# Optimization experiments

Measured on AMD Instinct MI355X. Metric: run time of the kernel, lower is better.

Reference implementation:

```python
import jax, jax.numpy as jnp
import numpy as np

KW, KH = 8, 8   # kernel_size = (kw, kh) per torch module indexing
SW, SH = 4, 4   # stride_size = (sw, sh)


def setup_inputs() -> dict:
    key = jax.random.key(0)
    x = jax.random.normal(key, (4, 128, 128, 128), dtype=jnp.float32)  # [B, C, H, W]
    return {"x": x}


def _local_autocorr(x, kh=KH, kw=KW, sh=SH, sw=SW):
    B, C, H, W = x.shape
    nh = (H - kh) // sh + 1
    nw = (W - kw) // sw + 1
    # Background is x zero-padded by (kh//2, (kh+1)//2 - 1) vertically and
    # (kw//2, (kw+1)//2 - 1) horizontally -> background patches are (2kh-1, 2kw-1).
    xp = jnp.pad(x, ((0, 0), (0, 0),
                     (kh // 2, (kh + 1) // 2 - 1),
                     (kw // 2, (kw + 1) // 2 - 1)))

    # For each shift (dy, dx) in [0,kh)x[0,kw):
    #   ret[b,iy,ix,c,dy,dx] = sum_{u,v} x[b,c,top+u,left+v] * xp[b,c,top+dy+u,left+dx+v]
    # i.e. elementwise product with the shifted map, then sum-pool with window (kh,kw), stride (sh,sw).
    def step(carry, s):
        dy = s // kw
        dx = s % kw
        shifted = jax.lax.dynamic_slice(xp, (0, 0, dy, dx), (B, C, H, W))
        prod = x * shifted
        pooled = jax.lax.reduce_window(prod, 0.0, jax.lax.add,
                                       (1, 1, kh, kw), (1, 1, sh, sw), 'VALID')
        return carry, pooled  # [B, C, nh, nw]

    _, stacked = jax.lax.scan(step, None, jnp.arange(kh * kw))
    # stacked: [kh*kw, B, C, nh, nw] with shift index s = dy*kw + dx
    out = stacked.reshape(kh, kw, B, C, nh, nw)
    out = jnp.transpose(out, (2, 4, 5, 3, 0, 1))  # [B, nh, nw, C, kh, kw]
    return out


def reference(x):
    return _local_autocorr(x)
```

## Files before the change

kernel.cpp:

```cpp
#include <hip/hip_runtime.h>


#define Cn 128
#define Hn 128
#define Wn 128
#define NH 31
#define NW 31
#define CB 4
#define PXT 8
#define PYT 4
#define TROWS 27
#define RST 44
#define CST (TROWS*RST)
#define F4C (TROWS*11)
#define TCST 17
#define TPST (CB*TCST+1)

__global__ __launch_bounds__(256, 2)
void lac_kernel(const float* __restrict__ x, float* __restrict__ out) {
    __shared__ float sm[CB * CST];

    const int bid = blockIdx.x;
    const int lg = ((bid & 7) << 9) | (bid >> 3);
    const int tx = lg & 3;
    const int ty = (lg >> 2) & 7;
    const int ct = (lg >> 5) & 31;
    const int b  = lg >> 10;
    const int c0 = ct * CB;
    const int gy0 = ty * (PYT * 4) - 4;
    const int gx0 = tx * (PXT * 4) - 4;
    const int tid = threadIdx.x;

    for (int i = tid; i < CB * F4C; i += 256) {
        const int c   = i / F4C;
        const int rem = i - c * F4C;
        const int r   = rem / 11;
        const int q   = rem - r * 11;
        const int y   = gy0 + r;
        const int xc  = gx0 + q * 4;
        const float* src = x + (((size_t)(b * Cn + c0 + c) * Hn + y) * Wn + xc);
        float4 v;
        if (y >= 0 && y < Hn && xc >= 0 && xc + 3 < Wn) {
            v = *reinterpret_cast<const float4*>(src);
        } else if (y >= 0 && y < Hn) {
            v.x = (xc + 0 >= 0 && xc + 0 < Wn) ? src[0] : 0.0f;
            v.y = (xc + 1 >= 0 && xc + 1 < Wn) ? src[1] : 0.0f;
            v.z = (xc + 2 >= 0 && xc + 2 < Wn) ? src[2] : 0.0f;
            v.w = (xc + 3 >= 0 && xc + 3 < Wn) ? src[3] : 0.0f;
        } else {
            v = make_float4(0.0f, 0.0f, 0.0f, 0.0f);
        }
        reinterpret_cast<float4*>(sm)[i] = v;
    }
    __syncthreads();

    const int cs   = tid & 3;
    const int px   = (tid >> 2) & 7;
    const int py   = (tid >> 5) & 3;
    const int half = tid >> 7;
    const float* rg  = &sm[cs * CST + (py * 4) * RST + px * 4];
    const float* rgr = rg + (half * 4) * RST;

    float acc[4][8];
#pragma unroll
    for (int i = 0; i < 4; ++i)
#pragma unroll
        for (int j = 0; j < 8; ++j) acc[i][j] = 0.0f;

#pragma unroll
    for (int rr = 0; rr < 11; ++rr) {
        float rw[16];
        float4 q0 = *reinterpret_cast<const float4*>(&rgr[rr * RST + 0]);
        float4 q1 = *reinterpret_cast<const float4*>(&rgr[rr * RST + 4]);
        float4 q2 = *reinterpret_cast<const float4*>(&rgr[rr * RST + 8]);
        float4 q3 = *reinterpret_cast<const float4*>(&rgr[rr * RST + 12]);
        rw[0]  = q0.x; rw[1]  = q0.y; rw[2]  = q0.z; rw[3]  = q0.w;
        rw[4]  = q1.x; rw[5]  = q1.y; rw[6]  = q1.z; rw[7]  = q1.w;
        rw[8]  = q2.x; rw[9]  = q2.y; rw[10] = q2.z; rw[11] = q2.w;
        rw[12] = q3.x; rw[13] = q3.y; rw[14] = q3.z; rw[15] = q3.w;
#pragma unroll
        for (int d = 0; d < 4; ++d) {
            const int u = rr - d;
            if (u >= 0 && u < 8) {
                float4 b0 = *reinterpret_cast<const float4*>(&rg[(u + 4) * RST + 4]);
                float4 b1 = *reinterpret_cast<const float4*>(&rg[(u + 4) * RST + 8]);
                float bsr[8];
                bsr[0] = b0.x; bsr[1] = b0.y; bsr[2] = b0.z; bsr[3] = b0.w;
                bsr[4] = b1.x; bsr[5] = b1.y; bsr[6] = b1.z; bsr[7] = b1.w;
#pragma unroll
                for (int v = 0; v < 8; ++v) {
                    const float bv = bsr[v];
#pragma unroll
                    for (int dx = 0; dx < 8; ++dx)
                        acc[d][dx] = fmaf(bv, rw[v + dx], acc[d][dx]);
                }
            }
        }
    }

    float4* lds4 = reinterpret_cast<float4*>(sm);
#pragma unroll
    for (int rnd = 0; rnd < 4; ++rnd) {
        __syncthreads();
        if (py == rnd) {
            const int wb = px * TPST + cs * TCST + half * 8;
#pragma unroll
            for (int d = 0; d < 4; ++d) {
                lds4[wb + d * 2 + 0] = make_float4(acc[d][0], acc[d][1], acc[d][2], acc[d][3]);
                lds4[wb + d * 2 + 1] = make_float4(acc[d][4], acc[d][5], acc[d][6], acc[d][7]);
            }
        }
        __syncthreads();
        const int iy = ty * PYT + rnd;
        if (iy < NH) {
#pragma unroll
            for (int sp = 0; sp < 2; ++sp) {
                const int p  = sp * 4 + (tid >> 6);
                const int ix = tx * PXT + p;
                if (ix < NW) {
                    const int j = tid & 63;
                    float4* obase = reinterpret_cast<float4*>(
                        out + ((((size_t)b * NH + iy) * NW + ix) * Cn + c0) * 64);
                    obase[j] = lds4[p * TPST + (j >> 4) * TCST + (j & 15)];
                }
            }
        }
    }
}

extern "C" void kernel_launch(void* const* d_in, const int* in_sizes, int n_in,
                              void* d_out, int out_size, void* d_ws, size_t ws_size,
                              hipStream_t stream) {
    const float* x = (const float*)d_in[0];
    float* out = (float*)d_out;
    lac_kernel<<<dim3(4096), dim3(256), 0, stream>>>(x, out);
}
```

Before: 101.4 us.

## Reuse loaded background rows as kernel rows via register ring buffer

```diff
diff --git a/kernel.cpp b/kernel.cpp
--- a/kernel.cpp
+++ b/kernel.cpp
@@ -11,14 +11,14 @@
 #define PYT 4
 #define TROWS 27
 #define RST 44
-#define CST (TROWS*RST)
+#define CSTF4 310
 #define F4C (TROWS*11)
 #define TCST 17
 #define TPST (CB*TCST+1)
 
 __global__ __launch_bounds__(256, 2)
 void lac_kernel(const float* __restrict__ x, float* __restrict__ out) {
-    __shared__ float sm[CB * CST];
+    __shared__ float sm[CB * CSTF4 * 4];
 
     const int bid = blockIdx.x;
     const int lg = ((bid & 7) << 9) | (bid >> 3);
@@ -50,7 +50,7 @@
         } else {
             v = make_float4(0.0f, 0.0f, 0.0f, 0.0f);
         }
-        reinterpret_cast<float4*>(sm)[i] = v;
+        reinterpret_cast<float4*>(sm)[c * CSTF4 + r * 11 + q] = v;
     }
     __syncthreads();
 
@@ -58,8 +58,7 @@
     const int px   = (tid >> 2) & 7;
     const int py   = (tid >> 5) & 3;
     const int half = tid >> 7;
-    const float* rg  = &sm[cs * CST + (py * 4) * RST + px * 4];
-    const float* rgr = rg + (half * 4) * RST;
+    const float* rg = &sm[cs * (CSTF4 * 4) + (py * 4) * RST + px * 4];
 
     float acc[4][8];
 #pragma unroll
@@ -67,36 +66,63 @@
 #pragma unroll
         for (int j = 0; j < 8; ++j) acc[i][j] = 0.0f;
 
+    float ks[4][8];
+
+#define LOAD_RW(R)                                                              \
+    float rw[16];                                                               \
+    {                                                                           \
+        float4 q0 = *reinterpret_cast<const float4*>(&rg[(R) * RST + 0]);       \
+        float4 q1 = *reinterpret_cast<const float4*>(&rg[(R) * RST + 4]);       \
+        float4 q2 = *reinterpret_cast<const float4*>(&rg[(R) * RST + 8]);       \
+        float4 q3 = *reinterpret_cast<const float4*>(&rg[(R) * RST + 12]);      \
+        rw[0]=q0.x; rw[1]=q0.y; rw[2]=q0.z; rw[3]=q0.w;                         \
+        rw[4]=q1.x; rw[5]=q1.y; rw[6]=q1.z; rw[7]=q1.w;                         \
+        rw[8]=q2.x; rw[9]=q2.y; rw[10]=q2.z; rw[11]=q2.w;                       \
+        rw[12]=q3.x; rw[13]=q3.y; rw[14]=q3.z; rw[15]=q3.w;                     \
+    }
+
+    if (half == 0) {
 #pragma unroll
-    for (int rr = 0; rr < 11; ++rr) {
-        float rw[16];
-        float4 q0 = *reinterpret_cast<const float4*>(&rgr[rr * RST + 0]);
-        float4 q1 = *reinterpret_cast<const float4*>(&rgr[rr * RST + 4]);
-        float4 q2 = *reinterpret_cast<const float4*>(&rgr[rr * RST + 8]);
-        float4 q3 = *reinterpret_cast<const float4*>(&rgr[rr * RST + 12]);
-        rw[0]  = q0.x; rw[1]  = q0.y; rw[2]  = q0.z; rw[3]  = q0.w;
-        rw[4]  = q1.x; rw[5]  = q1.y; rw[6]  = q1.z; rw[7]  = q1.w;
-        rw[8]  = q2.x; rw[9]  = q2.y; rw[10] = q2.z; rw[11] = q2.w;
-        rw[12] = q3.x; rw[13] = q3.y; rw[14] = q3.z; rw[15] = q3.w;
+        for (int ii = 0; ii < 12; ++ii) {
+            const int R = 11 - ii;
+            LOAD_RW(R)
 #pragma unroll
-        for (int d = 0; d < 4; ++d) {
-            const int u = rr - d;
-            if (u >= 0 && u < 8) {
-                float4 b0 = *reinterpret_cast<const float4*>(&rg[(u + 4) * RST + 4]);
-                float4 b1 = *reinterpret_cast<const float4*>(&rg[(u + 4) * RST + 8]);
-                float bsr[8];
-                bsr[0] = b0.x; bsr[1] = b0.y; bsr[2] = b0.z; bsr[3] = b0.w;
-                bsr[4] = b1.x; bsr[5] = b1.y; bsr[6] = b1.z; bsr[7] = b1.w;
+            for (int d = 0; d < 4; ++d) {
+                if (R >= d && R <= 7 + d) {
 #pragma unroll
-                for (int v = 0; v < 8; ++v) {
-                    const float bv = bsr[v];
+                    for (int v = 0; v < 8; ++v) {
+                        const float bv = ks[(R - d) & 3][v];
 #pragma unroll
-                    for (int dx = 0; dx < 8; ++dx)
-                        acc[d][dx] = fmaf(bv, rw[v + dx], acc[d][dx]);
+                        for (int dx = 0; dx < 8; ++dx)
+                            acc[d][dx] = fmaf(bv, rw[dx + v], acc[d][dx]);
+                    }
                 }
             }
+#pragma unroll
+            for (int v = 0; v < 8; ++v) ks[R & 3][v] = rw[4 + v];
+        }
+    } else {
+#pragma unroll
+        for (int ii = 0; ii < 11; ++ii) {
+            const int R = 4 + ii;
+            LOAD_RW(R)
+#pragma unroll
+            for (int d = 0; d < 4; ++d) {
+                if (R >= 4 + d && R <= 11 + d) {
+#pragma unroll
+                    for (int v = 0; v < 8; ++v) {
+                        const float bv = (d == 0) ? rw[4 + v] : ks[(R - d) & 3][v];
+#pragma unroll
+                        for (int dx = 0; dx < 8; ++dx)
+                            acc[d][dx] = fmaf(bv, rw[dx + v], acc[d][dx]);
+                    }
+                }
+            }
+#pragma unroll
+            for (int v = 0; v < 8; ++v) ks[R & 3][v] = rw[4 + v];
         }
     }
+#undef LOAD_RW
 
     float4* lds4 = reinterpret_cast<float4*>(sm);
 #pragma unroll
```

After: 81.09 us. 20.0% less time.
